# Kernel tuning notes

Hardware: AMD Instinct MI355X
Metric: run time of the kernel (lower is better)

The kernel has to match this reference:

```python
import jax, jax.numpy as jnp
import numpy as np

OUT_CH = 300
KSIZE = 337

def setup_inputs() -> dict:
    key = jax.random.key(0)
    k1, k2, kw, kb, kf1, kb1, kf2, kb2 = jax.random.split(key, 8)
    B, W = 512, 128
    x1 = jax.random.normal(k1, (B, W, KSIZE), dtype=jnp.float32)
    x2 = jax.random.normal(k2, (B, W, KSIZE), dtype=jnp.float32)
    # Conv1d(1, 300, 337) weight [300, 1, 337] -> collapse to [300, 337]
    conv_w = jax.random.normal(kw, (OUT_CH, KSIZE), dtype=jnp.float32) * (1.0 / np.sqrt(KSIZE))
    conv_b = jax.random.normal(kb, (OUT_CH,), dtype=jnp.float32) * 0.01
    fc1_w = jax.random.normal(kf1, (300, 600), dtype=jnp.float32) * (1.0 / np.sqrt(600))
    fc1_b = jax.random.normal(kb1, (300,), dtype=jnp.float32) * 0.01
    fc2_w = jax.random.normal(kf2, (1, 300), dtype=jnp.float32) * (1.0 / np.sqrt(300))
    fc2_b = jax.random.normal(kb2, (1,), dtype=jnp.float32) * 0.01
    return {"x1": x1, "x2": x2, "conv_w": conv_w, "conv_b": conv_b,
            "fc1_w": fc1_w, "fc1_b": fc1_b, "fc2_w": fc2_w, "fc2_b": fc2_b}

def _encode(x, conv_w, conv_b):
    # per-word conv1d with full-length kernel == matmul over last dim
    # x: [B, W, 337] -> [B, W, 300] -> relu -> max over words -> [B, 300]
    h = jnp.einsum('bwd,od->bwo', x, conv_w) + conv_b
    h = jax.nn.relu(h)
    return jnp.max(h, axis=1)

def reference(x1, x2, conv_w, conv_b, fc1_w, fc1_b, fc2_w, fc2_b):
    v1 = _encode(x1, conv_w, conv_b)
    v2 = _encode(x2, conv_w, conv_b)
    feat = jnp.concatenate([v1 - v2, v1 * v2], axis=1)  # [B, 600]
    h = jnp.tanh(feat @ fc1_w.T + fc1_b)
    return h @ fc2_w.T + fc2_b  # [B, 1]
```

## Files before the change

kernel.cpp:

```cpp
#include <hip/hip_runtime.h>
#include <hip/hip_fp16.h>
#include <stdint.h>


#define OC   300
#define OCP  320
#define KD   337
#define NBAT 512
#define NWRD 128
#define NKT  11
#define XSTR 36
#define XDW  (NWRD * XSTR)
#define BGR  1280

typedef _Float16 f16x8 __attribute__((ext_vector_type(8)));
typedef float    f32x4 __attribute__((ext_vector_type(4)));

#define GL_LDS(gp, lp, SZ)                                                        \
  __builtin_amdgcn_global_load_lds(                                               \
      (const __attribute__((address_space(1))) uint32_t*)(gp),                    \
      (__attribute__((address_space(3))) uint32_t*)(lp), SZ, 0, 0)

__global__ void prep_w_kernel(const float* __restrict__ cw, __half* __restrict__ Wp) {
  int i = blockIdx.x * 256 + threadIdx.x;
  if (i >= NKT * BGR) return;
  int kt = i / BGR, lin = i - kt * BGR;
  int o = lin >> 2, g = lin & 3;
  int slot = lin ^ (o & 7);
  __half h[8];
  #pragma unroll
  for (int e = 0; e < 8; ++e) {
    int k = kt * 32 + g * 8 + e;
    float v = (o < OC && k < KD) ? cw[o * KD + k] : 0.f;
    h[e] = __float2half(v);
  }
  *reinterpret_cast<uint4*>(Wp + (size_t)(kt * BGR + slot) * 8) =
      *reinterpret_cast<const uint4*>(h);
}

__global__ void prep_fc1t_kernel(const float* __restrict__ w, float* __restrict__ T) {
  int i = blockIdx.x * 256 + threadIdx.x;
  if (i >= 300 * 600) return;
  int j = i / 600, k = i - j * 600;
  T[k * 300 + j] = w[i];
}

__global__ __launch_bounds__(512, 4) void encode_gemm(
    const float* __restrict__ x1, const float* __restrict__ x2,
    const __half* __restrict__ Wp, const float* __restrict__ cb,
    float* __restrict__ V)
{
  __shared__ float Xt[2][XDW];
  __shared__ uint4 Bt[2][BGR];
  __shared__ float colmax[2][OCP];

  const int tid  = threadIdx.x;
  const int lane = tid & 63;
  const int wid  = tid >> 6;
  const int wm   = wid >> 2;
  const int wn   = wid & 3;
  const int ib   = blockIdx.x;
  const float* xb = (ib < NBAT ? x1 : x2) + (size_t)(ib & (NBAT - 1)) * (NWRD * KD);

  int rk[9];
  #pragma unroll
  for (int j = 0; j < 9; ++j) {
    int s = j * 512 + tid;
    int r = s / XSTR, k = s - r * XSTR;
    rk[j] = (r << 8) | ((k < 32) ? k : 31);
  }

  #define ISSUE(KT, BUF) do {                                                        \
    const int kt_ = (KT);                                                            \
    const int ko_ = kt_ * 32;                                                        \
    _Pragma("unroll")                                                                \
    for (int j = 0; j < 9; ++j) {                                                    \
      int r_ = rk[j] >> 8, kc_ = rk[j] & 255;                                        \
      int gk_ = ko_ + kc_; gk_ = (gk_ > KD - 1) ? (KD - 1) : gk_;    \
      GL_LDS(xb + (size_t)r_ * KD + gk_, &Xt[BUF][j * 512 + tid], 4);                \
    }                                                                                \
    const __half* wsrc_ = Wp + (size_t)kt_ * BGR * 8;                                \
    GL_LDS(wsrc_ + (size_t)tid * 8,          &Bt[BUF][tid],        16);              \
    GL_LDS(wsrc_ + (size_t)(tid + 512) * 8,  &Bt[BUF][tid + 512],  16);              \
    if (tid < 256)                                                                   \
      GL_LDS(wsrc_ + (size_t)(tid + 1024) * 8, &Bt[BUF][tid + 1024], 16);            \
  } while (0)

  f32x4 acc[4][5];
  #pragma unroll
  for (int mi = 0; mi < 4; ++mi)
    #pragma unroll
    for (int ni = 0; ni < 5; ++ni)
      acc[mi][ni] = (f32x4){0.f, 0.f, 0.f, 0.f};

  ISSUE(0, 0);
  asm volatile("s_waitcnt vmcnt(0)" ::: "memory");
  __syncthreads();

  const int k0 = (lane >> 4) * 8;
  for (int kt = 0; kt < NKT; ++kt) {
    const int cur = kt & 1;
    if (kt + 1 < NKT) ISSUE(kt + 1, cur ^ 1);

    f16x8 a[4];
    #pragma unroll
    for (int mi = 0; mi < 4; ++mi) {
      int r = wm * 64 + mi * 16 + (lane & 15);
      const float* xp = &Xt[cur][r * XSTR + k0];
      f32x4 lo = *reinterpret_cast<const f32x4*>(xp);
      f32x4 hi = *reinterpret_cast<const f32x4*>(xp + 4);
      f16x8 v;
      v[0] = (_Float16)lo[0]; v[1] = (_Float16)lo[1];
      v[2] = (_Float16)lo[2]; v[3] = (_Float16)lo[3];
      v[4] = (_Float16)hi[0]; v[5] = (_Float16)hi[1];
      v[6] = (_Float16)hi[2]; v[7] = (_Float16)hi[3];
      a[mi] = v;
    }
    #pragma unroll
    for (int ni = 0; ni < 5; ++ni) {
      int o    = wn * 80 + ni * 16 + (lane & 15);
      int slot = (o * 4 + (lane >> 4)) ^ (o & 7);
      f16x8 b = *reinterpret_cast<const f16x8*>(&Bt[cur][slot]);
      #pragma unroll
      for (int mi = 0; mi < 4; ++mi)
        acc[mi][ni] = __builtin_amdgcn_mfma_f32_16x16x32_f16(a[mi], b, acc[mi][ni], 0, 0, 0);
    }

    asm volatile("s_waitcnt vmcnt(0)" ::: "memory");
    __syncthreads();
  }

  #pragma unroll
  for (int ni = 0; ni < 5; ++ni) {
    float m = acc[0][ni][0];
    #pragma unroll
    for (int mi = 0; mi < 4; ++mi)
      #pragma unroll
      for (int j = 0; j < 4; ++j)
        m = fmaxf(m, acc[mi][ni][j]);
    m = fmaxf(m, __shfl_xor(m, 16));
    m = fmaxf(m, __shfl_xor(m, 32));
    if (lane < 16) colmax[wm][wn * 80 + ni * 16 + lane] = m;
  }
  __syncthreads();
  if (tid < OCP) {
    float v = fmaxf(colmax[0][tid], colmax[1][tid]);
    if (tid < OC) V[(size_t)ib * OC + tid] = fmaxf(v + cb[tid], 0.f);
  }
}

__global__ __launch_bounds__(320) void head_kernel(
    const float* __restrict__ V, const float* __restrict__ T,
    const float* __restrict__ fc1b, const float* __restrict__ fc2w,
    const float* __restrict__ fc2b, float* __restrict__ out)
{
  __shared__ float feat[8][600];
  __shared__ float partial[8][5];
  const int tid  = threadIdx.x;
  const int lane = tid & 63;
  const int wid  = tid >> 6;
  const int b0   = blockIdx.x * 8;

  for (int idx = tid; idx < 8 * 600; idx += 320) {
    int q = idx / 600, k = idx - q * 600;
    int b = b0 + q;
    int c = (k < 300) ? k : k - 300;
    float a1 = V[(size_t)b * OC + c];
    float a2 = V[(size_t)(NBAT + b) * OC + c];
    feat[q][k] = (k < 300) ? (a1 - a2) : (a1 * a2);
  }
  __syncthreads();

  const int j = tid;
  float h[8] = {0.f, 0.f, 0.f, 0.f, 0.f, 0.f, 0.f, 0.f};
  if (j < 300) {
    for (int k4 = 0; k4 < 150; ++k4) {
      float w0 = T[(k4 * 4 + 0) * 300 + j];
      float w1 = T[(k4 * 4 + 1) * 300 + j];
      float w2 = T[(k4 * 4 + 2) * 300 + j];
      float w3 = T[(k4 * 4 + 3) * 300 + j];
      #pragma unroll
      for (int q = 0; q < 8; ++q) {
        float4 fv = *reinterpret_cast<const float4*>(&feat[q][k4 * 4]);
        h[q] = fmaf(fv.x, w0, h[q]);
        h[q] = fmaf(fv.y, w1, h[q]);
        h[q] = fmaf(fv.z, w2, h[q]);
        h[q] = fmaf(fv.w, w3, h[q]);
      }
    }
  }
  float bias = (j < 300) ? fc1b[j] : 0.f;
  float w2j  = (j < 300) ? fc2w[j] : 0.f;
  #pragma unroll
  for (int q = 0; q < 8; ++q) {
    float g = (j < 300) ? tanhf(h[q] + bias) * w2j : 0.f;
    #pragma unroll
    for (int s = 1; s < 64; s <<= 1) g += __shfl_xor(g, s);
    if (lane == 0) partial[q][wid] = g;
  }
  __syncthreads();
  if (tid < 8) {
    float s = fc2b[0];
    #pragma unroll
    for (int wv = 0; wv < 5; ++wv) s += partial[tid][wv];
    out[b0 + tid] = s;
  }
}

extern "C" void kernel_launch(void* const* d_in, const int* in_sizes, int n_in,
                              void* d_out, int out_size, void* d_ws, size_t ws_size,
                              hipStream_t stream) {
  const float* x1     = (const float*)d_in[0];
  const float* x2     = (const float*)d_in[1];
  const float* conv_w = (const float*)d_in[2];
  const float* conv_b = (const float*)d_in[3];
  const float* fc1_w  = (const float*)d_in[4];
  const float* fc1_b  = (const float*)d_in[5];
  const float* fc2_w  = (const float*)d_in[6];
  const float* fc2_b  = (const float*)d_in[7];
  float* out = (float*)d_out;

  uint8_t* ws = (uint8_t*)d_ws;
  __half* Wp = (__half*)ws;
  float*  V  = (float*)(ws + 225280);
  float*  T  = (float*)(ws + 225280 + 1228800);

  prep_w_kernel<<<(NKT * BGR + 255) / 256, 256, 0, stream>>>(conv_w, Wp);
  prep_fc1t_kernel<<<(300 * 600 + 255) / 256, 256, 0, stream>>>(fc1_w, T);
  encode_gemm<<<1024, 512, 0, stream>>>(x1, x2, Wp, conv_b, V);
  head_kernel<<<64, 320, 0, stream>>>(V, T, fc1_b, fc2_w, fc2_b, out);
}
```

Measured before the change: 333.3 us.

## Split encoder GEMM across output halves, keep weights resident in LDS, load X directly to registers

The encoder kernel now launches two blocks per item, each covering half of the output channels. Each block loads its full 160-channel weight slice into LDS once, in an MFMA-fragment-friendly layout. X rows are read straight from global memory into registers with a two-stage register prefetch, replacing the LDS-staged double buffer and its per-tile barriers. Block indices are remapped so that both halves of an item land apart. This removes per-k-tile syncs and LDS traffic for X, but each X row is now read twice from global memory (relying on L2), and occupancy is lowered to 2 blocks.

```diff
diff --git a/kernel.cpp b/kernel.cpp
--- a/kernel.cpp
+++ b/kernel.cpp
@@ -3,15 +3,13 @@
 #include <stdint.h>
 
 
-#define OC   300
-#define OCP  320
-#define KD   337
-#define NBAT 512
-#define NWRD 128
-#define NKT  11
-#define XSTR 36
-#define XDW  (NWRD * XSTR)
-#define BGR  1280
+#define OC     300
+#define KD     337
+#define NBAT   512
+#define NWRD   128
+#define NKT    11
+#define NSTRIP 10
+#define NGR    (NKT * NSTRIP * 64)
 
 typedef _Float16 f16x8 __attribute__((ext_vector_type(8)));
 typedef float    f32x4 __attribute__((ext_vector_type(4)));
@@ -21,21 +19,25 @@
       (const __attribute__((address_space(1))) uint32_t*)(gp),                    \
       (__attribute__((address_space(3))) uint32_t*)(lp), SZ, 0, 0)
 
-__global__ void prep_w_kernel(const float* __restrict__ cw, __half* __restrict__ Wp) {
-  int i = blockIdx.x * 256 + threadIdx.x;
-  if (i >= NKT * BGR) return;
-  int kt = i / BGR, lin = i - kt * BGR;
-  int o = lin >> 2, g = lin & 3;
-  int slot = lin ^ (o & 7);
-  __half h[8];
+__global__ void prep_wf_kernel(const float* __restrict__ cw, __half* __restrict__ Wf) {
+  int g = blockIdx.x * 256 + threadIdx.x;
+  if (g >= 2 * NGR) return;
+  int lane  = g & 63;
+  int t     = g >> 6;
+  int strip = t % NSTRIP;
+  int hk    = t / NSTRIP;
+  int kt    = hk % NKT;
+  int nh    = hk / NKT;
+  int o     = nh * 160 + strip * 16 + (lane & 15);
+  int kb    = kt * 32 + (lane >> 4) * 8;
+  __half h8[8];
   #pragma unroll
   for (int e = 0; e < 8; ++e) {
-    int k = kt * 32 + g * 8 + e;
+    int k = kb + e;
     float v = (o < OC && k < KD) ? cw[o * KD + k] : 0.f;
-    h[e] = __float2half(v);
-  }
-  *reinterpret_cast<uint4*>(Wp + (size_t)(kt * BGR + slot) * 8) =
-      *reinterpret_cast<const uint4*>(h);
+    h8[e] = __float2half(v);
+  }
+  *reinterpret_cast<uint4*>(Wf + (size_t)g * 8) = *reinterpret_cast<const uint4*>(h8);
 }
 
 __global__ void prep_fc1t_kernel(const float* __restrict__ w, float* __restrict__ T) {
@@ -45,108 +47,137 @@
   T[k * 300 + j] = w[i];
 }
 
-__global__ __launch_bounds__(512, 4) void encode_gemm(
+__global__ __launch_bounds__(512, 2) void encode_gemm(
     const float* __restrict__ x1, const float* __restrict__ x2,
-    const __half* __restrict__ Wp, const float* __restrict__ cb,
+    const __half* __restrict__ Wf, const float* __restrict__ cb,
     float* __restrict__ V)
 {
-  __shared__ float Xt[2][XDW];
-  __shared__ uint4 Bt[2][BGR];
-  __shared__ float colmax[2][OCP];
+  __shared__ uint4 Blds[NGR];
+  __shared__ float colmax[4][160];
 
   const int tid  = threadIdx.x;
   const int lane = tid & 63;
   const int wid  = tid >> 6;
-  const int wm   = wid >> 2;
-  const int wn   = wid & 3;
-  const int ib   = blockIdx.x;
-  const float* xb = (ib < NBAT ? x1 : x2) + (size_t)(ib & (NBAT - 1)) * (NWRD * KD);
-
-  int rk[9];
-  #pragma unroll
-  for (int j = 0; j < 9; ++j) {
-    int s = j * 512 + tid;
-    int r = s / XSTR, k = s - r * XSTR;
-    rk[j] = (r << 8) | ((k < 32) ? k : 31);
-  }
-
-  #define ISSUE(KT, BUF) do {                                                        \
-    const int kt_ = (KT);                                                            \
-    const int ko_ = kt_ * 32;                                                        \
-    _Pragma("unroll")                                                                \
-    for (int j = 0; j < 9; ++j) {                                                    \
-      int r_ = rk[j] >> 8, kc_ = rk[j] & 255;                                        \
-      int gk_ = ko_ + kc_; gk_ = (gk_ > KD - 1) ? (KD - 1) : gk_;    \
-      GL_LDS(xb + (size_t)r_ * KD + gk_, &Xt[BUF][j * 512 + tid], 4);                \
-    }                                                                                \
-    const __half* wsrc_ = Wp + (size_t)kt_ * BGR * 8;                                \
-    GL_LDS(wsrc_ + (size_t)tid * 8,          &Bt[BUF][tid],        16);              \
-    GL_LDS(wsrc_ + (size_t)(tid + 512) * 8,  &Bt[BUF][tid + 512],  16);              \
-    if (tid < 256)                                                                   \
-      GL_LDS(wsrc_ + (size_t)(tid + 1024) * 8, &Bt[BUF][tid + 1024], 16);            \
-  } while (0)
-
-  f32x4 acc[4][5];
-  #pragma unroll
-  for (int mi = 0; mi < 4; ++mi)
+  const int wm   = wid >> 1;
+  const int wn   = wid & 1;
+
+  const int logical = ((blockIdx.x & 7) << 8) | (blockIdx.x >> 3);
+  const int item = logical >> 1;
+  const int nh   = logical & 1;
+
+  const float* xb = (item < NBAT ? x1 : x2) + (size_t)(item & (NBAT - 1)) * (NWRD * KD);
+
+  const __half* wsrc = Wf + (size_t)nh * NGR * 8;
+  #pragma unroll
+  for (int j = 0; j < 13; ++j)
+    GL_LDS(wsrc + (size_t)(j * 512 + tid) * 8, &Blds[j * 512 + tid], 16);
+  if (tid < 384)
+    GL_LDS(wsrc + (size_t)(13 * 512 + tid) * 8, &Blds[13 * 512 + tid], 16);
+
+  const int r0   = wm * 32 + (lane & 15);
+  const float* rp0 = xb + (size_t)r0 * KD;
+  const float* rp1 = rp0 + 16 * KD;
+  const int h4   = lane >> 4;
+  const int koct = h4 * 8;
+
+  f32x4 P0lo0, P0hi0, P0lo1, P0hi1;
+  f32x4 P1lo0, P1hi0, P1lo1, P1hi1;
+
+#define LOADA(KT, Alo0, Ahi0, Alo1, Ahi1) do {                        \
+    const float* p0_ = rp0 + (KT) * 32 + koct;                        \
+    const float* p1_ = rp1 + (KT) * 32 + koct;                        \
+    __builtin_memcpy(&Alo0, p0_,     16);                             \
+    __builtin_memcpy(&Ahi0, p0_ + 4, 16);                             \
+    __builtin_memcpy(&Alo1, p1_,     16);                             \
+    __builtin_memcpy(&Ahi1, p1_ + 4, 16);                             \
+  } while (0)
+
+#define LOADTAIL(Alo0, Ahi0, Alo1, Ahi1) do {                         \
+    if (h4 < 2) {                                                     \
+      const float* p0_ = rp0 + 320 + koct;                            \
+      const float* p1_ = rp1 + 320 + koct;                            \
+      __builtin_memcpy(&Alo0, p0_,     16);                           \
+      __builtin_memcpy(&Ahi0, p0_ + 4, 16);                           \
+      __builtin_memcpy(&Alo1, p1_,     16);                           \
+      __builtin_memcpy(&Ahi1, p1_ + 4, 16);                           \
+    } else {                                                          \
+      float s0_ = rp0[336], s1_ = rp1[336];                           \
+      Alo0 = (f32x4){s0_, s0_, s0_, s0_}; Ahi0 = Alo0;                \
+      Alo1 = (f32x4){s1_, s1_, s1_, s1_}; Ahi1 = Alo1;                \
+    }                                                                 \
+  } while (0)
+
+#define CVT2(Alo0, Ahi0, Alo1, Ahi1) do {                             \
+    a0[0] = (_Float16)Alo0[0]; a0[1] = (_Float16)Alo0[1];             \
+    a0[2] = (_Float16)Alo0[2]; a0[3] = (_Float16)Alo0[3];             \
+    a0[4] = (_Float16)Ahi0[0]; a0[5] = (_Float16)Ahi0[1];             \
+    a0[6] = (_Float16)Ahi0[2]; a0[7] = (_Float16)Ahi0[3];             \
+    a1[0] = (_Float16)Alo1[0]; a1[1] = (_Float16)Alo1[1];             \
+    a1[2] = (_Float16)Alo1[2]; a1[3] = (_Float16)Alo1[3];             \
+    a1[4] = (_Float16)Ahi1[0]; a1[5] = (_Float16)Ahi1[1];             \
+    a1[6] = (_Float16)Ahi1[2]; a1[7] = (_Float16)Ahi1[3];             \
+  } while (0)
+
+#define MFMAKT(KT) do {                                               \
+    _Pragma("unroll")                                                 \
+    for (int ni = 0; ni < 5; ++ni) {                                  \
+      f16x8 b_ = *reinterpret_cast<const f16x8*>(                     \
+          &Blds[((KT) * NSTRIP + wn * 5 + ni) * 64 + lane]);          \
+      acc[0][ni] = __builtin_amdgcn_mfma_f32_16x16x32_f16(a0, b_, acc[0][ni], 0, 0, 0); \
+      acc[1][ni] = __builtin_amdgcn_mfma_f32_16x16x32_f16(a1, b_, acc[1][ni], 0, 0, 0); \
+    }                                                                 \
+  } while (0)
+
+  f32x4 acc[2][5];
+  #pragma unroll
+  for (int mi = 0; mi < 2; ++mi)
     #pragma unroll
     for (int ni = 0; ni < 5; ++ni)
       acc[mi][ni] = (f32x4){0.f, 0.f, 0.f, 0.f};
 
-  ISSUE(0, 0);
+  LOADA(0, P0lo0, P0hi0, P0lo1, P0hi1);
+  LOADA(1, P1lo0, P1hi0, P1lo1, P1hi1);
+
   asm volatile("s_waitcnt vmcnt(0)" ::: "memory");
   __syncthreads();
 
-  const int k0 = (lane >> 4) * 8;
-  for (int kt = 0; kt < NKT; ++kt) {
-    const int cur = kt & 1;
-    if (kt + 1 < NKT) ISSUE(kt + 1, cur ^ 1);
-
-    f16x8 a[4];
-    #pragma unroll
-    for (int mi = 0; mi < 4; ++mi) {
-      int r = wm * 64 + mi * 16 + (lane & 15);
-      const float* xp = &Xt[cur][r * XSTR + k0];
-      f32x4 lo = *reinterpret_cast<const f32x4*>(xp);
-      f32x4 hi = *reinterpret_cast<const f32x4*>(xp + 4);
-      f16x8 v;
-      v[0] = (_Float16)lo[0]; v[1] = (_Float16)lo[1];
-      v[2] = (_Float16)lo[2]; v[3] = (_Float16)lo[3];
-      v[4] = (_Float16)hi[0]; v[5] = (_Float16)hi[1];
-      v[6] = (_Float16)hi[2]; v[7] = (_Float16)hi[3];
-      a[mi] = v;
-    }
-    #pragma unroll
-    for (int ni = 0; ni < 5; ++ni) {
-      int o    = wn * 80 + ni * 16 + (lane & 15);
-      int slot = (o * 4 + (lane >> 4)) ^ (o & 7);
-      f16x8 b = *reinterpret_cast<const f16x8*>(&Bt[cur][slot]);
-      #pragma unroll
-      for (int mi = 0; mi < 4; ++mi)
-        acc[mi][ni] = __builtin_amdgcn_mfma_f32_16x16x32_f16(a[mi], b, acc[mi][ni], 0, 0, 0);
-    }
-
-    asm volatile("s_waitcnt vmcnt(0)" ::: "memory");
-    __syncthreads();
-  }
+  f16x8 a0, a1;
+  #pragma unroll
+  for (int kt = 0; kt < 10; kt += 2) {
+    CVT2(P0lo0, P0hi0, P0lo1, P0hi1);
+    if (kt + 2 <= 9)       LOADA(kt + 2, P0lo0, P0hi0, P0lo1, P0hi1);
+    else                   LOADTAIL(P0lo0, P0hi0, P0lo1, P0hi1);
+    MFMAKT(kt);
+    CVT2(P1lo0, P1hi0, P1lo1, P1hi1);
+    if (kt + 3 <= 9)       LOADA(kt + 3, P1lo0, P1hi0, P1lo1, P1hi1);
+    MFMAKT(kt + 1);
+  }
+  CVT2(P0lo0, P0hi0, P0lo1, P0hi1);
+  MFMAKT(10);
 
   #pragma unroll
   for (int ni = 0; ni < 5; ++ni) {
-    float m = acc[0][ni][0];
-    #pragma unroll
-    for (int mi = 0; mi < 4; ++mi)
-      #pragma unroll
-      for (int j = 0; j < 4; ++j)
-        m = fmaxf(m, acc[mi][ni][j]);
+    float m = fmaxf(fmaxf(fmaxf(acc[0][ni][0], acc[0][ni][1]),
+                          fmaxf(acc[0][ni][2], acc[0][ni][3])),
+                    fmaxf(fmaxf(acc[1][ni][0], acc[1][ni][1]),
+                          fmaxf(acc[1][ni][2], acc[1][ni][3])));
     m = fmaxf(m, __shfl_xor(m, 16));
     m = fmaxf(m, __shfl_xor(m, 32));
     if (lane < 16) colmax[wm][wn * 80 + ni * 16 + lane] = m;
   }
   __syncthreads();
-  if (tid < OCP) {
-    float v = fmaxf(colmax[0][tid], colmax[1][tid]);
-    if (tid < OC) V[(size_t)ib * OC + tid] = fmaxf(v + cb[tid], 0.f);
-  }
+  if (tid < 160) {
+    int col = nh * 160 + tid;
+    if (col < OC) {
+      float v = fmaxf(fmaxf(colmax[0][tid], colmax[1][tid]),
+                      fmaxf(colmax[2][tid], colmax[3][tid]));
+      V[(size_t)item * OC + col] = fmaxf(v + cb[col], 0.f);
+    }
+  }
+#undef LOADA
+#undef LOADTAIL
+#undef CVT2
+#undef MFMAKT
 }
 
 __global__ __launch_bounds__(320) void head_kernel(
@@ -221,12 +252,12 @@
   float* out = (float*)d_out;
 
   uint8_t* ws = (uint8_t*)d_ws;
-  __half* Wp = (__half*)ws;
+  __half* Wf = (__half*)ws;
   float*  V  = (float*)(ws + 225280);
   float*  T  = (float*)(ws + 225280 + 1228800);
 
-  prep_w_kernel<<<(NKT * BGR + 255) / 256, 256, 0, stream>>>(conv_w, Wp);
+  prep_wf_kernel<<<(2 * NGR + 255) / 256, 256, 0, stream>>>(conv_w, Wf);
   prep_fc1t_kernel<<<(300 * 600 + 255) / 256, 256, 0, stream>>>(fc1_w, T);
-  encode_gemm<<<1024, 512, 0, stream>>>(x1, x2, Wp, conv_b, V);
+  encode_gemm<<<2048, 512, 0, stream>>>(x1, x2, Wf, conv_b, V);
   head_kernel<<<64, 320, 0, stream>>>(V, T, fc1_b, fc2_w, fc2_b, out);
 }
```

After: 313.1 us. 1.06x faster.
